# Optimization experiments

Measured on AMD Instinct MI355X. Metric: run time of the kernel, lower is better.

## Reference

```python
import jax, jax.numpy as jnp
import numpy as np

B, N, D, S = 4, 8, 64, 8192  # batch, heads, dim_head, seq_len


def setup_inputs() -> dict:
    key = jax.random.key(0)
    kq, kk, kv = jax.random.split(key, 3)
    q = jax.random.normal(kq, (B, N, D, S), dtype=jnp.float32)
    k = jax.random.normal(kk, (B, N, D, S), dtype=jnp.float32)
    v = jax.random.normal(kv, (B, N, D, S), dtype=jnp.float32)
    return {"q": q, "k": k, "v": v}


def reference(q, k, v):
    # q, k, v: [b, n, d, s] = [batch, heads, dim_head, seq]
    scale = q.shape[-2] ** -0.5  # dim_head^-0.5
    qs = jax.nn.softmax(q, axis=-2) * scale   # softmax over feature dim
    ks = jax.nn.softmax(k, axis=-1)           # softmax over seq dim
    # kv context: [b, n, d, d] -- avoids the O(s^2) score matrix
    context = jnp.einsum('bnis,bnjs->bnij', ks, v)
    # out: [b, n, d, s]
    return jnp.einsum('bnij,bnis->bnjs', context, qs)
```

## Files before the change

kernel.cpp:

```cpp
#include <hip/hip_runtime.h>
#include <math.h>


typedef _Float16 half8 __attribute__((ext_vector_type(8)));
typedef _Float16 half4v __attribute__((ext_vector_type(4)));
typedef float floatx4 __attribute__((ext_vector_type(4)));

constexpr int BHEADS = 32;
constexpr int DH     = 64;
constexpr int SEQ    = 8192;
constexpr float QSCALE = 0.125f;

__global__ __launch_bounds__(256)
void ctx_kernel(const float* __restrict__ K, const float* __restrict__ V,
                float* __restrict__ ctx, float* __restrict__ Z)
{
    const int head  = blockIdx.y;
    const int chunk = blockIdx.x;
    const int t     = threadIdx.x;
    const int lane  = t & 63;
    const int w     = t >> 6;
    const int ln    = lane & 15;
    const int q8    = lane >> 4;

    const float* kh = K + (size_t)head * DH * SEQ;
    const float* vh = V + (size_t)head * DH * SEQ;

    __shared__ __align__(16) _Float16 et[64 * 72];
    __shared__ __align__(16) _Float16 vt[64 * 72];
    __shared__ float zred[64 * 16];

    const int r0 = t >> 4;
    const int sc = 4 * (t & 15);
    const int s_blk = chunk * 256;

    float4 pk[4], pv[4];
    #pragma unroll
    for (int p = 0; p < 4; ++p) {
        const size_t off = (size_t)(r0 + 16 * p) * SEQ + s_blk + sc;
        pk[p] = *(const float4*)(kh + off);
        pv[p] = *(const float4*)(vh + off);
    }

    floatx4 acc[4];
    #pragma unroll
    for (int jt = 0; jt < 4; ++jt) acc[jt] = (floatx4){0.f, 0.f, 0.f, 0.f};
    float zacc[4] = {0.f, 0.f, 0.f, 0.f};

    for (int ts = 0; ts < 4; ++ts) {
        #pragma unroll
        for (int p = 0; p < 4; ++p) {
            const int i = r0 + 16 * p;
            const float e0 = __expf(pk[p].x), e1 = __expf(pk[p].y);
            const float e2 = __expf(pk[p].z), e3 = __expf(pk[p].w);
            zacc[p] += e0 + e1 + e2 + e3;
            *(half4v*)(et + i * 72 + sc) =
                (half4v){(_Float16)e0, (_Float16)e1, (_Float16)e2, (_Float16)e3};
            *(half4v*)(vt + i * 72 + sc) =
                (half4v){(_Float16)pv[p].x, (_Float16)pv[p].y,
                         (_Float16)pv[p].z, (_Float16)pv[p].w};
        }
        __syncthreads();
        if (ts < 3) {
            #pragma unroll
            for (int p = 0; p < 4; ++p) {
                const size_t off = (size_t)(r0 + 16 * p) * SEQ + s_blk + (ts + 1) * 64 + sc;
                pk[p] = *(const float4*)(kh + off);
                pv[p] = *(const float4*)(vh + off);
            }
        }
        #pragma unroll
        for (int st = 0; st < 2; ++st) {
            const half8 a = *(const half8*)(et + (16 * w + ln) * 72 + st * 32 + q8 * 8);
            #pragma unroll
            for (int jt = 0; jt < 4; ++jt) {
                const half8 b = *(const half8*)(vt + (16 * jt + ln) * 72 + st * 32 + q8 * 8);
                acc[jt] = __builtin_amdgcn_mfma_f32_16x16x32_f16(a, b, acc[jt], 0, 0, 0);
            }
        }
        __syncthreads();
    }

    float* ch = ctx + head * DH * DH;
    #pragma unroll
    for (int jt = 0; jt < 4; ++jt) {
        #pragma unroll
        for (int rr = 0; rr < 4; ++rr) {
            const int i = 16 * w + q8 * 4 + rr;
            const int j = 16 * jt + ln;
            unsafeAtomicAdd(&ch[i * DH + j], acc[jt][rr]);
        }
    }
    #pragma unroll
    for (int p = 0; p < 4; ++p) zred[(r0 + 16 * p) * 16 + (t & 15)] = zacc[p];
    __syncthreads();
    if (t < 64) {
        float z = 0.f;
        #pragma unroll
        for (int c = 0; c < 16; ++c) z += zred[t * 16 + c];
        unsafeAtomicAdd(&Z[head * DH + t], z);
    }
}

__global__ __launch_bounds__(256)
void out_kernel(const float* __restrict__ Q, const float* __restrict__ ctx,
                const float* __restrict__ Z, float* __restrict__ out)
{
    const int head = blockIdx.y;
    const int sb   = blockIdx.x;
    const int t    = threadIdx.x;
    const int lane = t & 63;
    const int w    = t >> 6;
    const int ln   = lane & 15;
    const int q8   = lane >> 4;

    __shared__ __align__(16) _Float16 czT[64 * 72];
    __shared__ __align__(16) float    qf[64 * 68];
    __shared__ __align__(16) _Float16 eqT[64 * 64];
    __shared__ float wred[64 * 4];
    __shared__ float rwsh[64];

    const float* qh = Q + (size_t)head * DH * SEQ;
    const int r0 = t >> 4;
    const int sc = 4 * (t & 15);
    const int s0 = sb * 256;

    float4 pq[4];
    #pragma unroll
    for (int p = 0; p < 4; ++p)
        pq[p] = *(const float4*)(qh + (size_t)(r0 + 16 * p) * SEQ + s0 + sc);

    {
        const float* ch = ctx + head * DH * DH;
        #pragma unroll
        for (int p = 0; p < 4; ++p) {
            const int i = r0 + 16 * p;
            const float rz = 1.0f / Z[head * DH + i];
            const float4 c4 = *(const float4*)(ch + i * DH + sc);
            czT[(sc + 0) * 72 + i] = (_Float16)(c4.x * rz);
            czT[(sc + 1) * 72 + i] = (_Float16)(c4.y * rz);
            czT[(sc + 2) * 72 + i] = (_Float16)(c4.z * rz);
            czT[(sc + 3) * 72 + i] = (_Float16)(c4.w * rz);
        }
    }
    __syncthreads();

    const half8 a0 = *(const half8*)(czT + (16 * w + ln) * 72 + 0 + q8 * 8);
    const half8 a1 = *(const half8*)(czT + (16 * w + ln) * 72 + 32 + q8 * 8);

    for (int r = 0; r < 4; ++r) {
        #pragma unroll
        for (int p = 0; p < 4; ++p)
            *(float4*)(qf + (r0 + 16 * p) * 68 + sc) = pq[p];
        __syncthreads();
        {
            const int s  = t & 63;
            const int cg = t >> 6;
            float wsum = 0.f;
            #pragma unroll
            for (int h = 0; h < 2; ++h) {
                const int cc = cg + 4 * h;
                half8 pk8;
                #pragma unroll
                for (int jj = 0; jj < 8; ++jj) {
                    const float e = __expf(qf[(8 * cc + jj) * 68 + s]);
                    wsum += e;
                    pk8[jj] = (_Float16)e;
                }
                *(half8*)(eqT + s * 64 + ((cc ^ (s & 7)) * 8)) = pk8;
            }
            wred[s * 4 + cg] = wsum;
        }
        __syncthreads();
        if (r < 3) {
            #pragma unroll
            for (int p = 0; p < 4; ++p)
                pq[p] = *(const float4*)(qh + (size_t)(r0 + 16 * p) * SEQ
                                         + s0 + (r + 1) * 64 + sc);
        }
        if (t < 64)
            rwsh[t] = QSCALE / (wred[t * 4] + wred[t * 4 + 1]
                                + wred[t * 4 + 2] + wred[t * 4 + 3]);
        floatx4 acc[4];
        #pragma unroll
        for (int nt = 0; nt < 4; ++nt) acc[nt] = (floatx4){0.f, 0.f, 0.f, 0.f};
        #pragma unroll
        for (int st = 0; st < 2; ++st) {
            const half8 a = (st == 0) ? a0 : a1;
            #pragma unroll
            for (int nt = 0; nt < 4; ++nt) {
                const int s  = 16 * nt + ln;
                const int cc = st * 4 + q8;
                const half8 b = *(const half8*)(eqT + s * 64 + ((cc ^ (s & 7)) * 8));
                acc[nt] = __builtin_amdgcn_mfma_f32_16x16x32_f16(a, b, acc[nt], 0, 0, 0);
            }
        }
        __syncthreads();
        float* oh = out + (size_t)head * DH * SEQ + s0 + r * 64;
        #pragma unroll
        for (int nt = 0; nt < 4; ++nt) {
            const int s = 16 * nt + ln;
            const float rw = rwsh[s];
            #pragma unroll
            for (int rr = 0; rr < 4; ++rr) {
                const int j = 16 * w + q8 * 4 + rr;
                oh[(size_t)j * SEQ + s] = acc[nt][rr] * rw;
            }
        }
    }
}

extern "C" void kernel_launch(void* const* d_in, const int* in_sizes, int n_in,
                              void* d_out, int out_size, void* d_ws, size_t ws_size,
                              hipStream_t stream)
{
    const float* q = (const float*)d_in[0];
    const float* k = (const float*)d_in[1];
    const float* v = (const float*)d_in[2];
    float* out = (float*)d_out;

    float* ctx = (float*)d_ws;
    float* Z   = ctx + BHEADS * DH * DH;

    const size_t zero_bytes = (size_t)(BHEADS * DH * DH + BHEADS * DH) * sizeof(float);
    hipMemsetAsync(d_ws, 0, zero_bytes, stream);

    ctx_kernel<<<dim3(32, BHEADS), 256, 0, stream>>>(k, v, ctx, Z);
    out_kernel<<<dim3(32, BHEADS), 256, 0, stream>>>(q, ctx, Z, out);
}
```

Baseline: 238.1 us.

## Replace atomic context accumulation with per-chunk partials and a reduce kernel

The context kernel now handles 512-sequence chunks (16 per head) and writes per-chunk partial context and normalizer sums to workspace instead of doing atomic adds. A new reduce kernel sums the partials, applies the 1/Z normalization and writes a transposed fp16 context once per head, so the output kernel no longer rebuilds it in every block. This also removes the memset. In exchange it adds a kernel launch, halves the context-kernel grid to 512 blocks, which lowers parallelism, and the output kernel drops one barrier while each thread computes the row weights itself.

```diff
diff --git a/kernel.cpp b/kernel.cpp
--- a/kernel.cpp
+++ b/kernel.cpp
@@ -3,17 +3,17 @@
 
 
 typedef _Float16 half8 __attribute__((ext_vector_type(8)));
-typedef _Float16 half4v __attribute__((ext_vector_type(4)));
 typedef float floatx4 __attribute__((ext_vector_type(4)));
 
 constexpr int BHEADS = 32;
 constexpr int DH     = 64;
 constexpr int SEQ    = 8192;
+constexpr int NCHUNK = 16;
 constexpr float QSCALE = 0.125f;
 
 __global__ __launch_bounds__(256)
-void ctx_kernel(const float* __restrict__ K, const float* __restrict__ V,
-                float* __restrict__ ctx, float* __restrict__ Z)
+void ctx_partial_kernel(const float* __restrict__ K, const float* __restrict__ V,
+                        float* __restrict__ partial, float* __restrict__ Zp)
 {
     const int head  = blockIdx.y;
     const int chunk = blockIdx.x;
@@ -28,45 +28,59 @@
 
     __shared__ __align__(16) _Float16 et[64 * 72];
     __shared__ __align__(16) _Float16 vt[64 * 72];
-    __shared__ float zred[64 * 16];
-
-    const int r0 = t >> 4;
-    const int sc = 4 * (t & 15);
-    const int s_blk = chunk * 256;
-
-    float4 pk[4], pv[4];
-    #pragma unroll
-    for (int p = 0; p < 4; ++p) {
-        const size_t off = (size_t)(r0 + 16 * p) * SEQ + s_blk + sc;
-        pk[p] = *(const float4*)(kh + off);
-        pv[p] = *(const float4*)(vh + off);
+    __shared__ __align__(16) float zred[64 * 8];
+
+    const int r0 = t >> 3;
+    const int c0 = 8 * (t & 7);
+    const int s_blk = chunk * 512;
+
+    float4 pk[2][2], pv[2][2];
+    #pragma unroll
+    for (int rr = 0; rr < 2; ++rr) {
+        const size_t base = (size_t)(r0 + 32 * rr) * SEQ + s_blk + c0;
+        pk[rr][0] = *(const float4*)(kh + base);
+        pk[rr][1] = *(const float4*)(kh + base + 4);
+        pv[rr][0] = *(const float4*)(vh + base);
+        pv[rr][1] = *(const float4*)(vh + base + 4);
     }
 
     floatx4 acc[4];
     #pragma unroll
     for (int jt = 0; jt < 4; ++jt) acc[jt] = (floatx4){0.f, 0.f, 0.f, 0.f};
-    float zacc[4] = {0.f, 0.f, 0.f, 0.f};
-
-    for (int ts = 0; ts < 4; ++ts) {
-        #pragma unroll
-        for (int p = 0; p < 4; ++p) {
-            const int i = r0 + 16 * p;
-            const float e0 = __expf(pk[p].x), e1 = __expf(pk[p].y);
-            const float e2 = __expf(pk[p].z), e3 = __expf(pk[p].w);
-            zacc[p] += e0 + e1 + e2 + e3;
-            *(half4v*)(et + i * 72 + sc) =
-                (half4v){(_Float16)e0, (_Float16)e1, (_Float16)e2, (_Float16)e3};
-            *(half4v*)(vt + i * 72 + sc) =
-                (half4v){(_Float16)pv[p].x, (_Float16)pv[p].y,
-                         (_Float16)pv[p].z, (_Float16)pv[p].w};
-        }
-        __syncthreads();
-        if (ts < 3) {
-            #pragma unroll
-            for (int p = 0; p < 4; ++p) {
-                const size_t off = (size_t)(r0 + 16 * p) * SEQ + s_blk + (ts + 1) * 64 + sc;
-                pk[p] = *(const float4*)(kh + off);
-                pv[p] = *(const float4*)(vh + off);
+    float zacc[2] = {0.f, 0.f};
+
+    for (int ts = 0; ts < 8; ++ts) {
+        #pragma unroll
+        for (int rr = 0; rr < 2; ++rr) {
+            const int row = r0 + 32 * rr;
+            float e[8];
+            e[0] = __expf(pk[rr][0].x); e[1] = __expf(pk[rr][0].y);
+            e[2] = __expf(pk[rr][0].z); e[3] = __expf(pk[rr][0].w);
+            e[4] = __expf(pk[rr][1].x); e[5] = __expf(pk[rr][1].y);
+            e[6] = __expf(pk[rr][1].z); e[7] = __expf(pk[rr][1].w);
+            zacc[rr] += e[0]+e[1]+e[2]+e[3]+e[4]+e[5]+e[6]+e[7];
+            half8 he, hv;
+            #pragma unroll
+            for (int x = 0; x < 4; ++x) {
+                he[x] = (_Float16)e[x]; he[x+4] = (_Float16)e[x+4];
+            }
+            hv[0] = (_Float16)pv[rr][0].x; hv[1] = (_Float16)pv[rr][0].y;
+            hv[2] = (_Float16)pv[rr][0].z; hv[3] = (_Float16)pv[rr][0].w;
+            hv[4] = (_Float16)pv[rr][1].x; hv[5] = (_Float16)pv[rr][1].y;
+            hv[6] = (_Float16)pv[rr][1].z; hv[7] = (_Float16)pv[rr][1].w;
+            *(half8*)(et + row * 72 + c0) = he;
+            *(half8*)(vt + row * 72 + c0) = hv;
+        }
+        __syncthreads();
+        if (ts < 7) {
+            #pragma unroll
+            for (int rr = 0; rr < 2; ++rr) {
+                const size_t base = (size_t)(r0 + 32 * rr) * SEQ + s_blk
+                                    + (ts + 1) * 64 + c0;
+                pk[rr][0] = *(const float4*)(kh + base);
+                pk[rr][1] = *(const float4*)(kh + base + 4);
+                pv[rr][0] = *(const float4*)(vh + base);
+                pv[rr][1] = *(const float4*)(vh + base + 4);
             }
         }
         #pragma unroll
@@ -81,30 +95,68 @@
         __syncthreads();
     }
 
-    float* ch = ctx + head * DH * DH;
+    float* ph = partial + (size_t)(head * NCHUNK + chunk) * DH * DH;
     #pragma unroll
     for (int jt = 0; jt < 4; ++jt) {
         #pragma unroll
         for (int rr = 0; rr < 4; ++rr) {
             const int i = 16 * w + q8 * 4 + rr;
             const int j = 16 * jt + ln;
-            unsafeAtomicAdd(&ch[i * DH + j], acc[jt][rr]);
-        }
-    }
-    #pragma unroll
-    for (int p = 0; p < 4; ++p) zred[(r0 + 16 * p) * 16 + (t & 15)] = zacc[p];
+            ph[i * DH + j] = acc[jt][rr];
+        }
+    }
+    zred[r0 * 8 + (t & 7)] = zacc[0];
+    zred[(r0 + 32) * 8 + (t & 7)] = zacc[1];
     __syncthreads();
     if (t < 64) {
+        const float4 z0 = *(const float4*)(zred + t * 8);
+        const float4 z1 = *(const float4*)(zred + t * 8 + 4);
+        Zp[(head * NCHUNK + chunk) * DH + t] =
+            z0.x + z0.y + z0.z + z0.w + z1.x + z1.y + z1.z + z1.w;
+    }
+}
+
+__global__ __launch_bounds__(256)
+void reduce_kernel(const float* __restrict__ partial, const float* __restrict__ Zp,
+                   _Float16* __restrict__ czT)
+{
+    const int h = blockIdx.x;
+    const int t = threadIdx.x;
+    __shared__ float rz[64];
+
+    if (t < 64) {
         float z = 0.f;
         #pragma unroll
-        for (int c = 0; c < 16; ++c) z += zred[t * 16 + c];
-        unsafeAtomicAdd(&Z[head * DH + t], z);
+        for (int c = 0; c < NCHUNK; ++c)
+            z += Zp[(h * NCHUNK + c) * DH + t];
+        rz[t] = 1.0f / z;
+    }
+    __syncthreads();
+
+    const float* ph = partial + (size_t)h * NCHUNK * DH * DH;
+    _Float16* ct = czT + (size_t)h * DH * DH;
+    #pragma unroll
+    for (int rep = 0; rep < 4; ++rep) {
+        const int idx = t + 256 * rep;
+        const int i   = idx >> 4;
+        const int j4  = idx & 15;
+        float4 sum = {0.f, 0.f, 0.f, 0.f};
+        #pragma unroll
+        for (int c = 0; c < NCHUNK; ++c) {
+            const float4 p = *(const float4*)(ph + (size_t)c * DH * DH + i * DH + j4 * 4);
+            sum.x += p.x; sum.y += p.y; sum.z += p.z; sum.w += p.w;
+        }
+        const float r = rz[i];
+        ct[(j4 * 4 + 0) * DH + i] = (_Float16)(sum.x * r);
+        ct[(j4 * 4 + 1) * DH + i] = (_Float16)(sum.y * r);
+        ct[(j4 * 4 + 2) * DH + i] = (_Float16)(sum.z * r);
+        ct[(j4 * 4 + 3) * DH + i] = (_Float16)(sum.w * r);
     }
 }
 
 __global__ __launch_bounds__(256)
-void out_kernel(const float* __restrict__ Q, const float* __restrict__ ctx,
-                const float* __restrict__ Z, float* __restrict__ out)
+void out_kernel(const float* __restrict__ Q, const _Float16* __restrict__ czT,
+                float* __restrict__ out)
 {
     const int head = blockIdx.y;
     const int sb   = blockIdx.x;
@@ -114,11 +166,9 @@
     const int ln   = lane & 15;
     const int q8   = lane >> 4;
 
-    __shared__ __align__(16) _Float16 czT[64 * 72];
     __shared__ __align__(16) float    qf[64 * 68];
     __shared__ __align__(16) _Float16 eqT[64 * 64];
-    __shared__ float wred[64 * 4];
-    __shared__ float rwsh[64];
+    __shared__ __align__(16) float    wred[64 * 4];
 
     const float* qh = Q + (size_t)head * DH * SEQ;
     const int r0 = t >> 4;
@@ -130,23 +180,9 @@
     for (int p = 0; p < 4; ++p)
         pq[p] = *(const float4*)(qh + (size_t)(r0 + 16 * p) * SEQ + s0 + sc);
 
-    {
-        const float* ch = ctx + head * DH * DH;
-        #pragma unroll
-        for (int p = 0; p < 4; ++p) {
-            const int i = r0 + 16 * p;
-            const float rz = 1.0f / Z[head * DH + i];
-            const float4 c4 = *(const float4*)(ch + i * DH + sc);
-            czT[(sc + 0) * 72 + i] = (_Float16)(c4.x * rz);
-            czT[(sc + 1) * 72 + i] = (_Float16)(c4.y * rz);
-            czT[(sc + 2) * 72 + i] = (_Float16)(c4.z * rz);
-            czT[(sc + 3) * 72 + i] = (_Float16)(c4.w * rz);
-        }
-    }
-    __syncthreads();
-
-    const half8 a0 = *(const half8*)(czT + (16 * w + ln) * 72 + 0 + q8 * 8);
-    const half8 a1 = *(const half8*)(czT + (16 * w + ln) * 72 + 32 + q8 * 8);
+    const _Float16* ch = czT + (size_t)head * DH * DH;
+    const half8 a0 = *(const half8*)(ch + (16 * w + ln) * DH + 0  + q8 * 8);
+    const half8 a1 = *(const half8*)(ch + (16 * w + ln) * DH + 32 + q8 * 8);
 
     for (int r = 0; r < 4; ++r) {
         #pragma unroll
@@ -158,29 +194,33 @@
             const int cg = t >> 6;
             float wsum = 0.f;
             #pragma unroll
-            for (int h = 0; h < 2; ++h) {
-                const int cc = cg + 4 * h;
-                half8 pk8;
+            for (int h2 = 0; h2 < 2; ++h2) {
+                const int cc = cg + 4 * h2;
+                half8 p8;
                 #pragma unroll
                 for (int jj = 0; jj < 8; ++jj) {
                     const float e = __expf(qf[(8 * cc + jj) * 68 + s]);
                     wsum += e;
-                    pk8[jj] = (_Float16)e;
+                    p8[jj] = (_Float16)e;
                 }
-                *(half8*)(eqT + s * 64 + ((cc ^ (s & 7)) * 8)) = pk8;
+                *(half8*)(eqT + s * 64 + ((cc ^ (s & 7)) * 8)) = p8;
             }
             wred[s * 4 + cg] = wsum;
         }
-        __syncthreads();
         if (r < 3) {
             #pragma unroll
             for (int p = 0; p < 4; ++p)
                 pq[p] = *(const float4*)(qh + (size_t)(r0 + 16 * p) * SEQ
                                          + s0 + (r + 1) * 64 + sc);
         }
-        if (t < 64)
-            rwsh[t] = QSCALE / (wred[t * 4] + wred[t * 4 + 1]
-                                + wred[t * 4 + 2] + wred[t * 4 + 3]);
+        __syncthreads();
+        float rw[4];
+        #pragma unroll
+        for (int nt = 0; nt < 4; ++nt) {
+            const int s2 = 16 * nt + ln;
+            const float4 wv = *(const float4*)(wred + s2 * 4);
+            rw[nt] = QSCALE / (wv.x + wv.y + wv.z + wv.w);
+        }
         floatx4 acc[4];
         #pragma unroll
         for (int nt = 0; nt < 4; ++nt) acc[nt] = (floatx4){0.f, 0.f, 0.f, 0.f};
@@ -189,22 +229,20 @@
             const half8 a = (st == 0) ? a0 : a1;
             #pragma unroll
             for (int nt = 0; nt < 4; ++nt) {
-                const int s  = 16 * nt + ln;
+                const int s2 = 16 * nt + ln;
                 const int cc = st * 4 + q8;
-                const half8 b = *(const half8*)(eqT + s * 64 + ((cc ^ (s & 7)) * 8));
+                const half8 b = *(const half8*)(eqT + s2 * 64 + ((cc ^ (s2 & 7)) * 8));
                 acc[nt] = __builtin_amdgcn_mfma_f32_16x16x32_f16(a, b, acc[nt], 0, 0, 0);
             }
         }
-        __syncthreads();
         float* oh = out + (size_t)head * DH * SEQ + s0 + r * 64;
         #pragma unroll
         for (int nt = 0; nt < 4; ++nt) {
-            const int s = 16 * nt + ln;
-            const float rw = rwsh[s];
+            const int s2 = 16 * nt + ln;
             #pragma unroll
             for (int rr = 0; rr < 4; ++rr) {
                 const int j = 16 * w + q8 * 4 + rr;
-                oh[(size_t)j * SEQ + s] = acc[nt][rr] * rw;
+                oh[(size_t)j * SEQ + s2] = acc[nt][rr] * rw[nt];
             }
         }
     }
@@ -219,12 +257,11 @@
     const float* v = (const float*)d_in[2];
     float* out = (float*)d_out;
 
-    float* ctx = (float*)d_ws;
-    float* Z   = ctx + BHEADS * DH * DH;
-
-    const size_t zero_bytes = (size_t)(BHEADS * DH * DH + BHEADS * DH) * sizeof(float);
-    hipMemsetAsync(d_ws, 0, zero_bytes, stream);
-
-    ctx_kernel<<<dim3(32, BHEADS), 256, 0, stream>>>(k, v, ctx, Z);
-    out_kernel<<<dim3(32, BHEADS), 256, 0, stream>>>(q, ctx, Z, out);
-}
+    float*    partial = (float*)d_ws;
+    float*    Zp      = partial + BHEADS * NCHUNK * DH * DH;
+    _Float16* czT     = (_Float16*)(Zp + BHEADS * NCHUNK * DH);
+
+    ctx_partial_kernel<<<dim3(NCHUNK, BHEADS), 256, 0, stream>>>(k, v, partial, Zp);
+    reduce_kernel<<<BHEADS, 256, 0, stream>>>(partial, Zp, czT);
+    out_kernel<<<dim3(32, BHEADS), 256, 0, stream>>>(q, czT, out);
+}
```

Result: no change. 238.7 us (+0.2%).
